# Kernel tuning notes

Measured on AMD Instinct MI355X. Metric: run time of the kernel, lower is better.

Reference implementation:

```python
import jax, jax.numpy as jnp
import numpy as np

EPS = 1e-5


def _ligru_layer(x, W, U, gamma, beta):
    """One bidirectional LiGRU layer. x: (B,T,F) -> (B,T,2H)."""
    B = x.shape[0]
    H = U.shape[1]
    # bidirectional: stack forward copy and time-flipped copy along batch
    x2 = jnp.concatenate([x, x[:, ::-1]], axis=0)  # (2B, T, F)
    w = jnp.einsum('btf,gf->btg', x2, W)           # (2B, T, 2H)
    # training-mode BatchNorm1d over flattened (2B*T, 2H), biased variance
    flat = w.reshape(-1, w.shape[-1])
    mean = flat.mean(axis=0)
    var = flat.var(axis=0)
    w = (w - mean) * jax.lax.rsqrt(var + EPS) * gamma + beta

    def step(h, wt):
        gates = wt + h @ U.T            # (2B, 2H)
        at, zt = gates[:, :H], gates[:, H:]
        z = jax.nn.sigmoid(zt)
        h = z * h + (1.0 - z) * jax.nn.relu(at)
        return h, h

    h0 = jnp.zeros((w.shape[0], H), dtype=w.dtype)
    _, hs = jax.lax.scan(step, h0, jnp.swapaxes(w, 0, 1))  # (T, 2B, H)
    hs = jnp.swapaxes(hs, 0, 1)                            # (2B, T, H)
    h_f, h_b = hs[:B], hs[B:, ::-1]                        # un-flip backward dir
    return jnp.concatenate([h_f, h_b], axis=2)             # (B, T, 2H)


def setup_inputs() -> dict:
    key = jax.random.key(0)
    ks = jax.random.split(key, 9)
    B, T, F, H = 16, 500, 512, 1024
    return {
        'x': jax.random.normal(ks[0], (B, T, F), jnp.float32),
        'w0': jax.random.normal(ks[1], (2 * H, F), jnp.float32) * (1.0 / np.sqrt(F)),
        'u0': jax.random.normal(ks[2], (2 * H, H), jnp.float32) * (1.0 / np.sqrt(H)),
        'g0': jax.random.uniform(ks[3], (2 * H,), jnp.float32, 0.5, 1.5),
        'b0': jax.random.normal(ks[4], (2 * H,), jnp.float32) * 0.1,
        'w1': jax.random.normal(ks[5], (2 * H, 2 * H), jnp.float32) * (1.0 / np.sqrt(2 * H)),
        'u1': jax.random.normal(ks[6], (2 * H, H), jnp.float32) * (1.0 / np.sqrt(H)),
        'g1': jax.random.uniform(ks[7], (2 * H,), jnp.float32, 0.5, 1.5),
        'b1': jax.random.normal(ks[8], (2 * H,), jnp.float32) * 0.1,
    }


def reference(x, w0, u0, g0, b0, w1, u1, g1, b1):
    h = _ligru_layer(x, w0, u0, g0, b0)   # (B, T, 2H)
    h = _ligru_layer(h, w1, u1, g1, b1)   # (B, T, 2H)
    return h
```

## Files before the change

kernel.cpp:

```cpp
#include <hip/hip_runtime.h>
#include <stdint.h>

#define KT 500
#define KH 1024
#define KG 2048

typedef short bf16x8 __attribute__((ext_vector_type(8)));
typedef float f32x4 __attribute__((ext_vector_type(4)));

__device__ __forceinline__ unsigned short f2bf(float f){
  union { float f; unsigned int i; } u; u.f = f;
  unsigned int x = u.i;
  return (unsigned short)((x + 0x7fffu + ((x >> 16) & 1u)) >> 16);
}
__device__ __forceinline__ float bf2f(unsigned short h){
  union { unsigned int i; float f; } u; u.i = ((unsigned int)h) << 16;
  return u.f;
}

__device__ __forceinline__ void load_b128_dev(uint4& dst, const void* p){
  asm volatile("global_load_dwordx4 %0, %1, off sc1"
               : "=v"(dst) : "v"(p) : "memory");
}
__device__ __forceinline__ void store_b32_dev(void* p, unsigned int v){
  asm volatile("global_store_dword %0, %1, off sc1"
               :: "v"(p), "v"(v) : "memory");
}
__device__ __forceinline__ void wait_vm0(){
  asm volatile("s_waitcnt vmcnt(0)" ::: "memory");
}

__global__ __launch_bounds__(256) void castk(const float* __restrict__ s,
                                             unsigned short* __restrict__ d, int n4){
  int i = blockIdx.x*256 + threadIdx.x;
  if (i >= n4) return;
  float4 v = ((const float4*)s)[i];
  unsigned int lo = (unsigned int)f2bf(v.x) | ((unsigned int)f2bf(v.y) << 16);
  unsigned int hi = (unsigned int)f2bf(v.z) | ((unsigned int)f2bf(v.w) << 16);
  ((uint2*)d)[i] = make_uint2(lo, hi);
}

template<int MODE, int KDIM>
__global__ __launch_bounds__(256) void gemm_bn(
    const unsigned short* __restrict__ A,
    const unsigned short* __restrict__ Bw,
    unsigned short* __restrict__ Wout)
{
  __shared__ __attribute__((aligned(16))) unsigned short As[128*72];
  __shared__ __attribute__((aligned(16))) unsigned short Bs[128*72];
  const int tid = threadIdx.x;
  const int lane = tid & 63, wid = tid >> 6;
  const int ntile = blockIdx.x, mtile = blockIdx.y;
  const int arow_loc = tid >> 3;
  const int k8 = tid & 7;

  long abaseLo[4], abaseHi[4], bbase[4];
  #pragma unroll
  for (int i = 0; i < 4; i++){
    int r = mtile*128 + i*32 + arow_loc;
    int s = r / KT;
    int t = r - s*KT;
    if (MODE == 0){
      abaseLo[i] = (s < 16) ? (long)((s*KT + t)*512)
                            : (long)(((s-16)*KT + (KT-1-t))*512);
      abaseHi[i] = 0;
    } else {
      int sp = s & 15;
      int rev = (s >= 16);
      abaseLo[i] = (long)((sp*KT + (rev ? KT-1-t : t)) * KH);
      abaseHi[i] = (long)(((16+sp)*KT + (rev ? t : KT-1-t)) * KH);
    }
    bbase[i] = (long)(ntile*128 + i*32 + arow_loc) * KDIM;
  }

  f32x4 acc[4][4];
  #pragma unroll
  for (int a=0;a<4;a++)
    #pragma unroll
    for (int b=0;b<4;b++)
      acc[a][b] = (f32x4){0.f,0.f,0.f,0.f};

  const int mhalf = wid & 1, nhalf = wid >> 1;
  const int lrow = lane & 15, quad = lane >> 4;

  for (int k0 = 0; k0 < KDIM; k0 += 64){
    const int kel = k0 + k8*8;
    #pragma unroll
    for (int i = 0; i < 4; i++){
      long aoff;
      if (MODE == 0) aoff = abaseLo[i] + kel;
      else           aoff = (kel < KH) ? (abaseLo[i] + kel) : (abaseHi[i] + (kel - KH));
      uint4 va = *(const uint4*)(A + aoff);
      uint4 vb = *(const uint4*)(Bw + bbase[i] + kel);
      *(uint4*)&As[(i*32 + arow_loc)*72 + k8*8] = va;
      *(uint4*)&Bs[(i*32 + arow_loc)*72 + k8*8] = vb;
    }
    __syncthreads();
    #pragma unroll
    for (int kk = 0; kk < 64; kk += 32){
      bf16x8 af[4], bfr[4];
      #pragma unroll
      for (int mt=0; mt<4; mt++)
        af[mt] = *(const bf16x8*)&As[(mhalf*64 + mt*16 + lrow)*72 + kk + quad*8];
      #pragma unroll
      for (int nt=0; nt<4; nt++)
        bfr[nt] = *(const bf16x8*)&Bs[(nhalf*64 + nt*16 + lrow)*72 + kk + quad*8];
      #pragma unroll
      for (int mt=0; mt<4; mt++)
        #pragma unroll
        for (int nt=0; nt<4; nt++)
          acc[mt][nt] = __builtin_amdgcn_mfma_f32_16x16x32_bf16(af[mt], bfr[nt], acc[mt][nt], 0, 0, 0);
    }
    __syncthreads();
  }

  #pragma unroll
  for (int mt=0; mt<4; mt++)
    #pragma unroll
    for (int nt=0; nt<4; nt++)
      #pragma unroll
      for (int r=0; r<4; r++){
        int grow = mtile*128 + mhalf*64 + mt*16 + quad*4 + r;
        int gcol = ntile*128 + nhalf*64 + nt*16 + lrow;
        Wout[(long)grow*KG + gcol] = f2bf(acc[mt][nt][r]);
      }
}

__global__ __launch_bounds__(256) void bn_partial(const unsigned short* __restrict__ W,
                                                  float* __restrict__ part){
  const int blk = blockIdx.x, tid = threadIdx.x;
  const int c0 = tid*8;
  float s[8], qq[8];
  #pragma unroll
  for (int j=0;j<8;j++){ s[j]=0.f; qq[j]=0.f; }
  const unsigned short* base = W + (long)blk*128*KG + c0;
  for (int r=0;r<128;r++){
    uint4 v = *(const uint4*)(base + (long)r*KG);
    unsigned int w[4] = {v.x, v.y, v.z, v.w};
    #pragma unroll
    for (int p=0;p<4;p++){
      union { unsigned int i; float f; } lo, hi;
      lo.i = w[p] << 16;
      hi.i = w[p] & 0xffff0000u;
      s[2*p]   += lo.f; qq[2*p]   += lo.f*lo.f;
      s[2*p+1] += hi.f; qq[2*p+1] += hi.f*hi.f;
    }
  }
  float* pd = part + (long)blk*4096;
  #pragma unroll
  for (int j=0;j<8;j++){ pd[c0+j] = s[j]; pd[KG + c0 + j] = qq[j]; }
}

__global__ __launch_bounds__(256) void bn_final(const float* __restrict__ part,
                                                const float* __restrict__ gamma,
                                                const float* __restrict__ beta,
                                                float* __restrict__ scsh){
  int g = blockIdx.x*256 + threadIdx.x;
  float s=0.f, qq=0.f;
  for (int b=0;b<125;b++){ s += part[(long)b*4096 + g]; qq += part[(long)b*4096 + KG + g]; }
  float mean = s * (1.f/16000.f);
  float var  = qq * (1.f/16000.f) - mean*mean;
  float sc = gamma[g] * rsqrtf(var + 1e-5f);
  scsh[g]      = sc;
  scsh[KG + g] = beta[g] - mean*sc;
}

template<int LAYER>
__global__ __launch_bounds__(256, 1) void recur(
    const unsigned short* __restrict__ Ub,
    const unsigned short* __restrict__ Wn,
    const float* __restrict__ scsh,
    unsigned short* __restrict__ hbuf,
    int* __restrict__ flags,
    unsigned short* __restrict__ hsOut,
    float* __restrict__ out)
{
  __shared__ __attribute__((aligned(16))) unsigned short Ush[32*1032];
  __shared__ __attribute__((aligned(16))) unsigned short hsh[32*1032];
  __shared__ float gA[32*20];
  __shared__ float gZ[32*20];
  __shared__ float hown[512];
  __shared__ float scA[16], shA[16], scZ[16], shZ[16];

  const int tid = threadIdx.x;
  const int q = blockIdx.x;
  const int ga = q*16;

  #pragma unroll
  for (int i=0;i<16;i++){
    int c = i*256 + tid;
    int row = c >> 7, k8c = c & 127;
    int grow = (row < 16) ? (ga + row) : (KH + ga + row - 16);
    uint4 v = *(const uint4*)(Ub + (long)grow*KH + k8c*8);
    *(uint4*)&Ush[row*1032 + k8c*8] = v;
  }
  if (tid < 64){
    int j = tid & 15, w = tid >> 4;
    if      (w==0) scA[j] = scsh[ga+j];
    else if (w==1) shA[j] = scsh[KG + ga + j];
    else if (w==2) scZ[j] = scsh[KH + ga + j];
    else           shZ[j] = scsh[KG + KH + ga + j];
  }
  hown[tid] = 0.f; hown[tid+256] = 0.f;
  __syncthreads();

  const int lane = tid & 63, wid = tid >> 6;
  const int lrow = lane & 15, quad = lane >> 4;
  const int mhalf = wid & 1, ghalf = wid >> 1;
  const int es = tid >> 3, ep = tid & 7;
  const int r0 = tid >> 7, kc = tid & 127;

  for (int t = 0; t < KT; t++){
    const unsigned short* wr = Wn + (long)(es*KT + t)*KG + ga + 2*ep;
    unsigned int wa01 = *(const unsigned int*)(wr);
    unsigned int wz01 = *(const unsigned int*)(wr + KH);
    asm volatile("" ::: "memory");

    if (t > 0 && tid < 64){
      while (__hip_atomic_load(&flags[(t-1)*64 + tid], __ATOMIC_RELAXED,
                               __HIP_MEMORY_SCOPE_AGENT) == 0){}
    }
    __syncthreads();

    const unsigned short* hb = hbuf + (t & 1)*32768 + r0*KH + kc*8;
    uint4 hreg[16];
    #pragma unroll
    for (int i=0;i<16;i++)
      load_b128_dev(hreg[i], hb + i*2048);
    wait_vm0();
    #pragma unroll
    for (int i=0;i<16;i++)
      *(uint4*)&hsh[(2*i + r0)*1032 + kc*8] = hreg[i];
    __syncthreads();

    f32x4 a0 = (f32x4){0,0,0,0}, a1 = a0, a2 = a0, a3 = a0;
    const unsigned short* ar = &hsh[(mhalf*16 + lrow)*1032 + quad*8];
    const unsigned short* br = &Ush[(ghalf*16 + lrow)*1032 + quad*8];
    #pragma unroll
    for (int k0=0;k0<KH;k0+=128){
      a0 = __builtin_amdgcn_mfma_f32_16x16x32_bf16(*(const bf16x8*)(ar+k0),    *(const bf16x8*)(br+k0),    a0,0,0,0);
      a1 = __builtin_amdgcn_mfma_f32_16x16x32_bf16(*(const bf16x8*)(ar+k0+32), *(const bf16x8*)(br+k0+32), a1,0,0,0);
      a2 = __builtin_amdgcn_mfma_f32_16x16x32_bf16(*(const bf16x8*)(ar+k0+64), *(const bf16x8*)(br+k0+64), a2,0,0,0);
      a3 = __builtin_amdgcn_mfma_f32_16x16x32_bf16(*(const bf16x8*)(ar+k0+96), *(const bf16x8*)(br+k0+96), a3,0,0,0);
    }
    f32x4 accs = (a0 + a1) + (a2 + a3);
    float* gd = ghalf ? gZ : gA;
    #pragma unroll
    for (int r=0;r<4;r++)
      gd[(mhalf*16 + quad*4 + r)*20 + lrow] = accs[r];
    __syncthreads();

    float2 gav = *(const float2*)&gA[es*20 + 2*ep];
    float2 gzv = *(const float2*)&gZ[es*20 + 2*ep];
    float2 hpv = *(const float2*)&hown[es*16 + 2*ep];
    float2 scav = *(const float2*)&scA[2*ep];
    float2 shav = *(const float2*)&shA[2*ep];
    float2 sczv = *(const float2*)&scZ[2*ep];
    float2 shzv = *(const float2*)&shZ[2*ep];
    float aa0 = gav.x + bf2f((unsigned short)(wa01 & 0xffff)) * scav.x + shav.x;
    float aa1 = gav.y + bf2f((unsigned short)(wa01 >> 16))    * scav.y + shav.y;
    float zz0 = gzv.x + bf2f((unsigned short)(wz01 & 0xffff)) * sczv.x + shzv.x;
    float zz1 = gzv.y + bf2f((unsigned short)(wz01 >> 16))    * sczv.y + shzv.y;
    float z0 = 1.f/(1.f + __expf(-zz0));
    float z1 = 1.f/(1.f + __expf(-zz1));
    float hn0 = z0*hpv.x + (1.f - z0)*fmaxf(aa0, 0.f);
    float hn1 = z1*hpv.y + (1.f - z1)*fmaxf(aa1, 0.f);
    *(float2*)&hown[es*16 + 2*ep] = make_float2(hn0, hn1);

    unsigned int hpack = (unsigned int)f2bf(hn0) | ((unsigned int)f2bf(hn1) << 16);
    store_b32_dev(hbuf + ((t+1)&1)*32768 + es*KH + ga + 2*ep, hpack);
    wait_vm0();
    __syncthreads();
    if (tid == 0)
      __hip_atomic_store(&flags[t*64 + q], 1, __ATOMIC_RELAXED, __HIP_MEMORY_SCOPE_AGENT);

    if (LAYER == 0){
      *(unsigned int*)&hsOut[(long)(es*KT + t)*KH + ga + 2*ep] = hpack;
    } else {
      if (es < 16)
        *(float2*)&out[(long)(es*KT + t)*KG + ga + 2*ep] = make_float2(hn0, hn1);
      else
        *(float2*)&out[(long)((es-16)*KT + (KT-1-t))*KG + KH + ga + 2*ep] = make_float2(hn0, hn1);
    }
  }
}

extern "C" void kernel_launch(void* const* d_in, const int* in_sizes, int n_in,
                              void* d_out, int out_size, void* d_ws, size_t ws_size,
                              hipStream_t stream)
{
  const float* x  = (const float*)d_in[0];
  const float* w0 = (const float*)d_in[1];
  const float* u0 = (const float*)d_in[2];
  const float* g0 = (const float*)d_in[3];
  const float* b0 = (const float*)d_in[4];
  const float* w1 = (const float*)d_in[5];
  const float* u1 = (const float*)d_in[6];
  const float* g1 = (const float*)d_in[7];
  const float* b1 = (const float*)d_in[8];
  float* out = (float*)d_out;

  char* p = (char*)d_ws;
  auto alloc = [&](size_t n){ char* r = p; p += (n + 255) & ~(size_t)255; return r; };
  unsigned short* xb   = (unsigned short*)alloc((size_t)16*KT*512*2);
  unsigned short* w0b  = (unsigned short*)alloc((size_t)KG*512*2);
  unsigned short* u0b  = (unsigned short*)alloc((size_t)KG*KH*2);
  unsigned short* w1b  = (unsigned short*)alloc((size_t)KG*KG*2);
  unsigned short* u1b  = (unsigned short*)alloc((size_t)KG*KH*2);
  unsigned short* wbuf = (unsigned short*)alloc((size_t)32*KT*KG*2);
  unsigned short* hs0  = (unsigned short*)alloc((size_t)32*KT*KH*2);
  float* part          = (float*)alloc((size_t)125*4096*4);
  float* scsh          = (float*)alloc((size_t)2*KG*4);
  unsigned short* hbuf = (unsigned short*)alloc((size_t)2*2*32*KH*2);
  int* flags           = (int*)alloc((size_t)2*KT*64*4);

  auto cast = [&](const float* s, unsigned short* d, int n){
    int n4 = n >> 2;
    castk<<<(n4+255)/256, 256, 0, stream>>>(s, d, n4);
  };
  cast(x,  xb,  16*KT*512);
  cast(w0, w0b, KG*512);
  cast(u0, u0b, KG*KH);
  cast(w1, w1b, KG*KG);
  cast(u1, u1b, KG*KH);
  hipMemsetAsync(hbuf,  0, (size_t)2*2*32*KH*2, stream);
  hipMemsetAsync(flags, 0, (size_t)2*KT*64*4,  stream);

  gemm_bn<0,512><<<dim3(16,125), 256, 0, stream>>>(xb, w0b, wbuf);
  bn_partial<<<125,256,0,stream>>>(wbuf, part);
  bn_final<<<8,256,0,stream>>>(part, g0, b0, scsh);
  recur<0><<<64,256,0,stream>>>(u0b, wbuf, scsh, hbuf, flags, hs0, (float*)nullptr);

  gemm_bn<1,2048><<<dim3(16,125), 256, 0, stream>>>(hs0, w1b, wbuf);
  bn_partial<<<125,256,0,stream>>>(wbuf, part);
  bn_final<<<8,256,0,stream>>>(part, g1, b1, scsh);
  recur<1><<<64,256,0,stream>>>(u1b, wbuf, scsh, hbuf + 2*32*KH, flags + KT*64,
                                (unsigned short*)nullptr, out);
}
```

Measured before the change: 4.570 ms.

## Replace per-step flag barrier with tagged hidden-state words for inter-block sync

Each bf16 hidden value is now stored in a 32-bit word together with a 16-bit timestep tag, so consumer blocks poll the h buffer directly and retry only chunks whose tag is stale. This removes the flag array, the store-wait-barrier-flag-store sequence and the separate spin-then-barrier before loading h. The cost is a doubled h buffer and load traffic, more registers for 32 outstanding loads, and reliance on 8-byte stores being seen atomically.

```diff
diff --git a/kernel.cpp b/kernel.cpp
--- a/kernel.cpp
+++ b/kernel.cpp
@@ -18,16 +18,13 @@
   return u.f;
 }
 
-__device__ __forceinline__ void load_b128_dev(uint4& dst, const void* p){
-  asm volatile("global_load_dwordx4 %0, %1, off sc1"
-               : "=v"(dst) : "v"(p) : "memory");
-}
-__device__ __forceinline__ void store_b32_dev(void* p, unsigned int v){
-  asm volatile("global_store_dword %0, %1, off sc1"
-               :: "v"(p), "v"(v) : "memory");
-}
-__device__ __forceinline__ void wait_vm0(){
-  asm volatile("s_waitcnt vmcnt(0)" ::: "memory");
+__device__ __forceinline__ uint4 load_b128_vol(const void* p){
+  uint4 d;
+  asm volatile("global_load_dwordx4 %0, %1, off sc1" : "=v"(d) : "v"(p));
+  return d;
+}
+__device__ __forceinline__ void store_b64_dev(void* p, uint2 v){
+  asm volatile("global_store_dwordx2 %0, %1, off sc1" :: "v"(p), "v"(v));
 }
 
 __global__ __launch_bounds__(256) void castk(const float* __restrict__ s,
@@ -170,8 +167,7 @@
     const unsigned short* __restrict__ Ub,
     const unsigned short* __restrict__ Wn,
     const float* __restrict__ scsh,
-    unsigned short* __restrict__ hbuf,
-    int* __restrict__ flags,
+    unsigned int* __restrict__ hbuf32,
     unsigned short* __restrict__ hsOut,
     float* __restrict__ out)
 {
@@ -208,29 +204,49 @@
   const int lrow = lane & 15, quad = lane >> 4;
   const int mhalf = wid & 1, ghalf = wid >> 1;
   const int es = tid >> 3, ep = tid & 7;
-  const int r0 = tid >> 7, kc = tid & 127;
 
   for (int t = 0; t < KT; t++){
+    const unsigned int T = (unsigned int)t;
+    const unsigned int tagpair = T | (T << 16);
+
     const unsigned short* wr = Wn + (long)(es*KT + t)*KG + ga + 2*ep;
     unsigned int wa01 = *(const unsigned int*)(wr);
     unsigned int wz01 = *(const unsigned int*)(wr + KH);
     asm volatile("" ::: "memory");
 
-    if (t > 0 && tid < 64){
-      while (__hip_atomic_load(&flags[(t-1)*64 + tid], __ATOMIC_RELAXED,
-                               __HIP_MEMORY_SCOPE_AGENT) == 0){}
-    }
-    __syncthreads();
-
-    const unsigned short* hb = hbuf + (t & 1)*32768 + r0*KH + kc*8;
-    uint4 hreg[16];
-    #pragma unroll
-    for (int i=0;i<16;i++)
-      load_b128_dev(hreg[i], hb + i*2048);
-    wait_vm0();
-    #pragma unroll
-    for (int i=0;i<16;i++)
-      *(uint4*)&hsh[(2*i + r0)*1032 + kc*8] = hreg[i];
+    const unsigned int* hb = hbuf32 + (size_t)(t & 1)*32768 + 4*tid;
+    uint4 v[32];
+    #pragma unroll
+    for (int i=0;i<32;i++)
+      v[i] = load_b128_vol(hb + (size_t)i*1024);
+    unsigned int pend = 0u;
+    #pragma unroll
+    for (int i=0;i<32;i++){
+      unsigned int t01 = __builtin_amdgcn_perm(v[i].y, v[i].x, 0x07060302u);
+      unsigned int t23 = __builtin_amdgcn_perm(v[i].w, v[i].z, 0x07060302u);
+      if (t01 == tagpair && t23 == tagpair){
+        unsigned int p01 = __builtin_amdgcn_perm(v[i].y, v[i].x, 0x05040100u);
+        unsigned int p23 = __builtin_amdgcn_perm(v[i].w, v[i].z, 0x05040100u);
+        *(uint2*)&hsh[i*1032 + 4*tid] = make_uint2(p01, p23);
+      } else pend |= (1u << i);
+    }
+    while (__builtin_expect(pend != 0u, 0)){
+      #pragma unroll
+      for (int i=0;i<32;i++)
+        if (pend & (1u<<i)) v[i] = load_b128_vol(hb + (size_t)i*1024);
+      #pragma unroll
+      for (int i=0;i<32;i++)
+        if (pend & (1u<<i)){
+          unsigned int t01 = __builtin_amdgcn_perm(v[i].y, v[i].x, 0x07060302u);
+          unsigned int t23 = __builtin_amdgcn_perm(v[i].w, v[i].z, 0x07060302u);
+          if (t01 == tagpair && t23 == tagpair){
+            unsigned int p01 = __builtin_amdgcn_perm(v[i].y, v[i].x, 0x05040100u);
+            unsigned int p23 = __builtin_amdgcn_perm(v[i].w, v[i].z, 0x05040100u);
+            *(uint2*)&hsh[i*1032 + 4*tid] = make_uint2(p01, p23);
+            pend &= ~(1u<<i);
+          }
+        }
+    }
     __syncthreads();
 
     f32x4 a0 = (f32x4){0,0,0,0}, a1 = a0, a2 = a0, a3 = a0;
@@ -265,16 +281,16 @@
     float z1 = 1.f/(1.f + __expf(-zz1));
     float hn0 = z0*hpv.x + (1.f - z0)*fmaxf(aa0, 0.f);
     float hn1 = z1*hpv.y + (1.f - z1)*fmaxf(aa1, 0.f);
+
+    unsigned short hb0 = f2bf(hn0), hb1 = f2bf(hn1);
+    unsigned int tagn = (T + 1u) << 16;
+    store_b64_dev((void*)(hbuf32 + (size_t)((t+1)&1)*32768 + es*1024 + ga + 2*ep),
+                  make_uint2((unsigned int)hb0 | tagn, (unsigned int)hb1 | tagn));
+
     *(float2*)&hown[es*16 + 2*ep] = make_float2(hn0, hn1);
 
-    unsigned int hpack = (unsigned int)f2bf(hn0) | ((unsigned int)f2bf(hn1) << 16);
-    store_b32_dev(hbuf + ((t+1)&1)*32768 + es*KH + ga + 2*ep, hpack);
-    wait_vm0();
-    __syncthreads();
-    if (tid == 0)
-      __hip_atomic_store(&flags[t*64 + q], 1, __ATOMIC_RELAXED, __HIP_MEMORY_SCOPE_AGENT);
-
     if (LAYER == 0){
+      unsigned int hpack = (unsigned int)hb0 | ((unsigned int)hb1 << 16);
       *(unsigned int*)&hsOut[(long)(es*KT + t)*KH + ga + 2*ep] = hpack;
     } else {
       if (es < 16)
@@ -311,8 +327,7 @@
   unsigned short* hs0  = (unsigned short*)alloc((size_t)32*KT*KH*2);
   float* part          = (float*)alloc((size_t)125*4096*4);
   float* scsh          = (float*)alloc((size_t)2*KG*4);
-  unsigned short* hbuf = (unsigned short*)alloc((size_t)2*2*32*KH*2);
-  int* flags           = (int*)alloc((size_t)2*KT*64*4);
+  unsigned int* hbuf   = (unsigned int*)alloc((size_t)2*2*32768*4);
 
   auto cast = [&](const float* s, unsigned short* d, int n){
     int n4 = n >> 2;
@@ -323,17 +338,16 @@
   cast(u0, u0b, KG*KH);
   cast(w1, w1b, KG*KG);
   cast(u1, u1b, KG*KH);
-  hipMemsetAsync(hbuf,  0, (size_t)2*2*32*KH*2, stream);
-  hipMemsetAsync(flags, 0, (size_t)2*KT*64*4,  stream);
+  hipMemsetAsync(hbuf, 0, (size_t)2*2*32768*4, stream);
 
   gemm_bn<0,512><<<dim3(16,125), 256, 0, stream>>>(xb, w0b, wbuf);
   bn_partial<<<125,256,0,stream>>>(wbuf, part);
   bn_final<<<8,256,0,stream>>>(part, g0, b0, scsh);
-  recur<0><<<64,256,0,stream>>>(u0b, wbuf, scsh, hbuf, flags, hs0, (float*)nullptr);
+  recur<0><<<64,256,0,stream>>>(u0b, wbuf, scsh, hbuf, hs0, (float*)nullptr);
 
   gemm_bn<1,2048><<<dim3(16,125), 256, 0, stream>>>(hs0, w1b, wbuf);
   bn_partial<<<125,256,0,stream>>>(wbuf, part);
   bn_final<<<8,256,0,stream>>>(part, g1, b1, scsh);
-  recur<1><<<64,256,0,stream>>>(u1b, wbuf, scsh, hbuf + 2*32*KH, flags + KT*64,
+  recur<1><<<64,256,0,stream>>>(u1b, wbuf, scsh, hbuf + 2*32768,
                                 (unsigned short*)nullptr, out);
 }
```

Measured after the change: 5.933 ms. 1.3x slower.
